# Performance work log

Measured on AMD Instinct MI355X. Metric: run time of the kernel, lower is better.

## Reference

```python
import jax, jax.numpy as jnp
import numpy as np

B, S, E, H = 4, 4096, 256, 2048
EPS = 1e-5

def layernorm(x, g, b):
    mu = jnp.mean(x, axis=-1, keepdims=True)
    var = jnp.mean(jnp.square(x - mu), axis=-1, keepdims=True)
    return (x - mu) * jax.lax.rsqrt(var + EPS) * g + b

def setup_inputs() -> dict:
    key = jax.random.key(0)
    ks = jax.random.split(key, 16)
    sE = 1.0 / np.sqrt(E)
    sH = 1.0 / np.sqrt(H)
    return {
        "x_embeddings": jax.random.normal(ks[0], (B, S, E), dtype=jnp.float32),
        "wq": jax.random.normal(ks[1], (E, E), dtype=jnp.float32) * sE,
        "bq": jnp.zeros((E,), jnp.float32),
        "wk": jax.random.normal(ks[2], (E, E), dtype=jnp.float32) * sE,
        "bk": jnp.zeros((E,), jnp.float32),
        "wv": jax.random.normal(ks[3], (E, E), dtype=jnp.float32) * sE,
        "bv": jnp.zeros((E,), jnp.float32),
        "w0": jax.random.normal(ks[4], (E, E), dtype=jnp.float32) * sE,
        "b0": jnp.zeros((E,), jnp.float32),
        "w1": jax.random.normal(ks[5], (E, H), dtype=jnp.float32) * sE,
        "b1": jnp.zeros((H,), jnp.float32),
        "ln_mlp_g": jnp.ones((H,), jnp.float32),
        "ln_mlp_b": jnp.zeros((H,), jnp.float32),
        "w2": jax.random.normal(ks[6], (H, E), dtype=jnp.float32) * sH,
        "b2": jnp.zeros((E,), jnp.float32),
        "ln1_g": jnp.ones((E,), jnp.float32),
        "ln1_b": jnp.zeros((E,), jnp.float32),
        "ln2_g": jnp.ones((E,), jnp.float32),
        "ln2_b": jnp.zeros((E,), jnp.float32),
    }

def reference(x_embeddings, wq, bq, wk, bk, wv, bv, w0, b0,
              w1, b1, ln_mlp_g, ln_mlp_b, w2, b2,
              ln1_g, ln1_b, ln2_g, ln2_b):
    x = x_embeddings
    q = x @ wq + bq
    k = x @ wk + bk
    v = x @ wv + bv
    # Unscaled, unmasked attention (faithful to source: no 1/sqrt(d), mask unused)
    scores = jnp.einsum('bqd,bkd->bqk', q, k)          # [B,S,S]
    probs = jax.nn.softmax(scores, axis=-1)
    attn = jnp.einsum('bqk,bkd->bqd', probs, v)        # [B,S,E]
    e = layernorm(x + attn, ln1_g, ln1_b) @ w0 + b0
    h = e @ w1 + b1                                     # [B,S,H]
    h = jax.nn.leaky_relu(layernorm(h, ln_mlp_g, ln_mlp_b))  # LnActivation: LN + LeakyReLU
    logits = h @ w2 + b2                                # [B,S,E]
    return layernorm(jax.nn.leaky_relu(logits + e), ln2_g, ln2_b)
```

## Files before the change

kernel.cpp:

```cpp
#include <hip/hip_runtime.h>

typedef unsigned short u16;
typedef unsigned int   u32;
typedef u16   u16x4 __attribute__((ext_vector_type(4)));
typedef u16   u16x8 __attribute__((ext_vector_type(8)));
typedef short s16x8 __attribute__((ext_vector_type(8)));
typedef float f32x4 __attribute__((ext_vector_type(4)));
typedef _Float16 f16x8 __attribute__((ext_vector_type(8)));

__device__ __forceinline__ u16 f2b(float f) {
  u32 u = __builtin_bit_cast(u32, f);
  u32 r = (u + 0x7fffu + ((u >> 16) & 1u)) >> 16;
  return (u16)r;
}
__device__ __forceinline__ float b2f(u16 h) {
  return __builtin_bit_cast(float, (u32)h << 16);
}
__device__ __forceinline__ u16 f2h(float f) {
  _Float16 h = (_Float16)f;
  return __builtin_bit_cast(u16, h);
}

__device__ __forceinline__ void async16(void* l, const void* g) {
  __builtin_amdgcn_global_load_lds((const __attribute__((address_space(1))) u32*)g,
                                   (__attribute__((address_space(3))) u32*)l, 16, 0, 0);
}

__device__ __forceinline__ float wave_sum(float v) {
#pragma unroll
  for (int m = 32; m; m >>= 1) v += __shfl_xor(v, m, 64);
  return v;
}

constexpr int BM = 128, BN = 128, BK = 64;

template<bool SPLIT, int OMODE>
__global__ __launch_bounds__(256)
void k_gemm_bt(const u16* __restrict__ Ah, const u16* __restrict__ Al, long lda,
               const u16* __restrict__ Bh, const u16* __restrict__ Bl, long ldb,
               const float* __restrict__ bias,
               float* __restrict__ Cf, u16* __restrict__ Cb, u16* __restrict__ Cl,
               long ldc, int K)
{
  __shared__ u16 lds[(SPLIT ? 4 : 2) * BM * BK];
  const int tid = threadIdx.x;
  const long arow0 = (long)blockIdx.y * BM;
  const long bcol0 = (long)blockIdx.x * BN;

  long offA[4], offB[4];
#pragma unroll
  for (int r = 0; r < 4; ++r) {
    const int off = r * 4096 + tid * 16;
    const int row = off >> 7;
    const int colb = off & 127;
    offA[r] = (arow0 + row) * lda + (colb >> 1);
    offB[r] = (bcol0 + row) * ldb + (colb >> 1);
  }

  const int lane = tid & 63;
  const int wid = tid >> 6;
  const int wr = (wid >> 1) * 64;
  const int wc = (wid & 1) * 64;
  const int fr = lane & 15;
  const int fk = (lane >> 4) * 8;

  f32x4 acc[4][4] = {};

  for (int k0 = 0; k0 < K; k0 += BK) {
#pragma unroll
    for (int r = 0; r < 4; ++r) {
      const int loff = (r * 4096 + tid * 16) >> 1;
      async16(&lds[loff],           Ah + offA[r] + k0);
      async16(&lds[BM*BK + loff],   Bh + offB[r] + k0);
      if constexpr (SPLIT) {
        async16(&lds[2*BM*BK + loff], Al + offA[r] + k0);
        async16(&lds[3*BM*BK + loff], Bl + offB[r] + k0);
      }
    }
    __syncthreads();
#pragma unroll
    for (int kk = 0; kk < BK; kk += 32) {
      s16x8 a[4], b[4];
#pragma unroll
      for (int m = 0; m < 4; ++m)
        a[m] = *(const s16x8*)&lds[(wr + m*16 + fr) * BK + kk + fk];
#pragma unroll
      for (int n = 0; n < 4; ++n)
        b[n] = *(const s16x8*)&lds[BM*BK + (wc + n*16 + fr) * BK + kk + fk];
#pragma unroll
      for (int m = 0; m < 4; ++m)
#pragma unroll
        for (int n = 0; n < 4; ++n)
          acc[m][n] = __builtin_amdgcn_mfma_f32_16x16x32_bf16(a[m], b[n], acc[m][n], 0, 0, 0);
      if constexpr (SPLIT) {
        s16x8 al[4], bl[4];
#pragma unroll
        for (int m = 0; m < 4; ++m)
          al[m] = *(const s16x8*)&lds[2*BM*BK + (wr + m*16 + fr) * BK + kk + fk];
#pragma unroll
        for (int n = 0; n < 4; ++n)
          bl[n] = *(const s16x8*)&lds[3*BM*BK + (wc + n*16 + fr) * BK + kk + fk];
#pragma unroll
        for (int m = 0; m < 4; ++m)
#pragma unroll
          for (int n = 0; n < 4; ++n) {
            acc[m][n] = __builtin_amdgcn_mfma_f32_16x16x32_bf16(a[m], bl[n], acc[m][n], 0, 0, 0);
            acc[m][n] = __builtin_amdgcn_mfma_f32_16x16x32_bf16(al[m], b[n], acc[m][n], 0, 0, 0);
          }
      }
    }
    __syncthreads();
  }

  float bv[4];
#pragma unroll
  for (int n = 0; n < 4; ++n) {
    const long gcol = bcol0 + wc + n*16 + fr;
    bv[n] = bias ? bias[gcol] : 0.f;
  }

#pragma unroll
  for (int m = 0; m < 4; ++m) {
#pragma unroll
    for (int reg = 0; reg < 4; ++reg) {
      const long grow = arow0 + wr + m*16 + (lane >> 4) * 4 + reg;
      const long ro = grow * ldc;
#pragma unroll
      for (int n = 0; n < 4; ++n) {
        const long gcol = bcol0 + wc + n*16 + fr;
        const float val = acc[m][n][reg] + bv[n];
        if constexpr (OMODE == 0) {
          Cf[ro + gcol] = val;
        } else if constexpr (OMODE == 1) {
          Cb[ro + gcol] = f2b(val);
        } else if constexpr (OMODE == 4) {
          Cb[ro + gcol] = f2h(val);
        } else if constexpr (OMODE == 5) {
          const int band = (int)(bcol0 >> 8);
          u16* dst = (band == 0) ? Cb : (band == 1) ? Cl : (u16*)Cf;
          const long lc = gcol - (long)band * 256;
          dst[grow * 256 + lc] = (band < 2) ? f2h(val) : f2b(val);
        } else {
          const u16 hb = f2b(val);
          Cb[ro + gcol] = hb;
          Cl[ro + gcol] = f2b(val - b2f(hb));
        }
      }
    }
  }
}

__global__ __launch_bounds__(256)
void k_flash(const u16* __restrict__ q16, const u16* __restrict__ k16,
             const u16* __restrict__ vt,
             u16* __restrict__ attn)
{
  __shared__ u16 lkh[2][32*256];
  __shared__ float lS[32*36];
  __shared__ u16 lP[32*40];
  __shared__ float lm[32], ll[32], lsc[32];

  const int tid = threadIdx.x;
  const int lane = tid & 63, wid = tid >> 6;
  const long bo = (long)blockIdx.y * 1048576;
  const long q0 = (long)blockIdx.x * 32;

  const int fr  = lane & 15;
  const int hi2 = lane >> 4;
  const int fk  = hi2 * 8;
  const int qh_sel = wid >> 1;
  const int kh_sel = wid & 1;

  f16x8 qf[8];
  {
    const u16* qp = q16 + bo + (q0 + qh_sel*16 + fr) * 256;
#pragma unroll
    for (int c = 0; c < 8; ++c)
      qf[c] = *(const f16x8*)(qp + c*32 + fk);
  }

  if (tid < 32) { lm[tid] = -1e30f; ll[tid] = 0.f; }
  f32x4 acc[2][4] = {};

  const char* kp = (const char*)(k16 + bo);
  const u16* vbase = vt + bo;

  auto STAGE = [&](int k0s, int b) {
#pragma unroll
    for (int r = 0; r < 4; ++r) {
      const int L = r*4096 + tid*16;
      const int row = L >> 9;
      const int colb = L & 511;
      const long gb = (long)(k0s + row)*512 + (colb ^ ((row & 7) << 4));
      async16((char*)lkh[b] + L, kp + gb);
    }
  };

  STAGE(0, 0);
  __syncthreads();

  int cur = 0;
  for (int k0 = 0; k0 < 4096; k0 += 32) {
    s16x8 vb[4];
#pragma unroll
    for (int j = 0; j < 4; ++j)
      vb[j] = *(const s16x8*)(vbase + (long)(wid*64 + j*16 + fr)*4096 + k0 + fk);

    if (k0 + 32 < 4096) STAGE(k0 + 32, cur ^ 1);

    f32x4 s0 = {};
    const int kc = kh_sel*16 + fr;
    const int swz = (kc & 7) << 4;
#pragma unroll
    for (int c = 0; c < 8; ++c) {
      const int o = (c*64 + hi2*16) ^ swz;
      const f16x8 bh = *(const f16x8*)((const char*)lkh[cur] + kc*512 + o);
      s0 = __builtin_amdgcn_mfma_f32_16x16x32_f16(qf[c], bh, s0, 0, 0, 0);
    }
#pragma unroll
    for (int r = 0; r < 4; ++r)
      lS[(qh_sel*16 + hi2*4 + r)*36 + kh_sel*16 + fr] = s0[r];
    __syncthreads();

    {
      const int sr = tid >> 3;
      const int sc = (tid & 7) * 4;
      const float4 sv = *(const float4*)&lS[sr*36 + sc];
      float tmx = fmaxf(fmaxf(sv.x, sv.y), fmaxf(sv.z, sv.w));
#pragma unroll
      for (int m = 1; m < 8; m <<= 1) tmx = fmaxf(tmx, __shfl_xor(tmx, m, 64));
      const float mold = lm[sr];
      const float mnew = fmaxf(mold, tmx);
      const float p0 = __expf(sv.x - mnew), p1 = __expf(sv.y - mnew);
      const float p2 = __expf(sv.z - mnew), p3 = __expf(sv.w - mnew);
      float ps = p0 + p1 + p2 + p3;
#pragma unroll
      for (int m = 1; m < 8; m <<= 1) ps += __shfl_xor(ps, m, 64);
      const float scale = __expf(mold - mnew);
      if ((tid & 7) == 0) {
        lm[sr] = mnew;
        ll[sr] = ll[sr] * scale + ps;
        lsc[sr] = scale;
      }
      u16x4 pb; pb[0]=f2b(p0); pb[1]=f2b(p1); pb[2]=f2b(p2); pb[3]=f2b(p3);
      *(u16x4*)&lP[sr*40 + sc] = pb;
    }
    __syncthreads();

#pragma unroll
    for (int qm = 0; qm < 2; ++qm)
#pragma unroll
      for (int r = 0; r < 4; ++r) {
        const float s = lsc[qm*16 + hi2*4 + r];
#pragma unroll
        for (int j = 0; j < 4; ++j) acc[qm][j][r] *= s;
      }
#pragma unroll
    for (int qm = 0; qm < 2; ++qm) {
      const s16x8 pa = *(const s16x8*)&lP[(qm*16 + fr)*40 + fk];
#pragma unroll
      for (int j = 0; j < 4; ++j)
        acc[qm][j] = __builtin_amdgcn_mfma_f32_16x16x32_bf16(pa, vb[j], acc[qm][j], 0, 0, 0);
    }
    cur ^= 1;
  }

  __syncthreads();
#pragma unroll
  for (int qm = 0; qm < 2; ++qm)
#pragma unroll
    for (int r = 0; r < 4; ++r) {
      const int row = qm*16 + hi2*4 + r;
      const float inv = 1.0f / ll[row];
      u16* op = attn + bo + (q0 + row)*256 + wid*64 + fr;
#pragma unroll
      for (int j = 0; j < 4; ++j)
        op[j*16] = f2b(acc[qm][j][r] * inv);
    }
}


__global__ __launch_bounds__(256)
void k_split_cast(const float* __restrict__ in, u16* __restrict__ hi, u16* __restrict__ lo, long n4) {
  long i = (long)blockIdx.x * 256 + threadIdx.x;
  if (i >= n4) return;
  float4 v = ((const float4*)in)[i];
  float vv[4] = {v.x, v.y, v.z, v.w};
  u16x4 h, l;
#pragma unroll
  for (int j = 0; j < 4; ++j) {
    u16 hb = f2b(vv[j]);
    h[j] = hb;
    l[j] = f2b(vv[j] - b2f(hb));
  }
  ((u16x4*)hi)[i] = h;
  ((u16x4*)lo)[i] = l;
}

__global__ __launch_bounds__(256)
void k_transpose_qkv0(const float* __restrict__ wq, const float* __restrict__ wk,
                      const float* __restrict__ wv, const float* __restrict__ w0,
                      u16* __restrict__ catT_h, u16* __restrict__ catT_l,
                      u16* __restrict__ w0T,
                      const float* __restrict__ bq, const float* __restrict__ bk,
                      const float* __restrict__ bv, float* __restrict__ catBias) {
  __shared__ float t[32][33];
  const int z = blockIdx.z;
  const float* in = (z == 0) ? wq : (z == 1) ? wk : (z == 2) ? wv : w0;
  const int c0 = blockIdx.x * 32, r0 = blockIdx.y * 32;
  const int tx = threadIdx.x, ty = threadIdx.y;
#pragma unroll
  for (int i = 0; i < 4; ++i)
    t[ty + i*8][tx] = in[(long)(r0 + ty + i*8) * 256 + c0 + tx];
  __syncthreads();
#pragma unroll
  for (int i = 0; i < 4; ++i) {
    const float f = t[tx][ty + i*8];
    const u16 hb = f2b(f);
    if (z < 3) {
      const long o = (long)(z*256 + c0 + ty + i*8) * 256 + r0 + tx;
      catT_h[o] = hb;
      catT_l[o] = f2b(f - b2f(hb));
    } else {
      w0T[(long)(c0 + ty + i*8) * 256 + r0 + tx] = hb;
    }
  }
  if (z == 3 && blockIdx.x == 0 && blockIdx.y == 0) {
    const int t0 = ty * 32 + tx;
    catBias[t0] = bq[t0];
    catBias[256 + t0] = bk[t0];
    catBias[512 + t0] = bv[t0];
  }
}

__global__ __launch_bounds__(256)
void k_transpose_f32ns(const float* __restrict__ in, u16* __restrict__ hi, int R, int C) {
  __shared__ float t[32][33];
  const int c0 = blockIdx.x * 32, r0 = blockIdx.y * 32;
  const int tx = threadIdx.x, ty = threadIdx.y;
#pragma unroll
  for (int i = 0; i < 4; ++i)
    t[ty + i*8][tx] = in[(long)(r0 + ty + i*8) * C + c0 + tx];
  __syncthreads();
#pragma unroll
  for (int i = 0; i < 4; ++i)
    hi[(long)(c0 + ty + i*8) * R + r0 + tx] = f2b(t[tx][ty + i*8]);
}

__global__ __launch_bounds__(256)
void k_transpose_bf16(const u16* __restrict__ in, u16* __restrict__ out,
                      int R, int C, long sIn, long sOut) {
  __shared__ u16 t[32][34];
  const int z = blockIdx.z;
  const u16* ib = in + (long)z * sIn;
  u16* ob = out + (long)z * sOut;
  const int c0 = blockIdx.x * 32, r0 = blockIdx.y * 32;
  const int tx = threadIdx.x, ty = threadIdx.y;
#pragma unroll
  for (int i = 0; i < 4; ++i)
    t[ty + i*8][tx] = ib[(long)(r0 + ty + i*8) * C + c0 + tx];
  __syncthreads();
#pragma unroll
  for (int i = 0; i < 4; ++i)
    ob[(long)(c0 + ty + i*8) * R + r0 + tx] = t[tx][ty + i*8];
}

__global__ __launch_bounds__(256)
void k_add_ln(const float* __restrict__ x, const u16* __restrict__ a,
              const float* __restrict__ g, const float* __restrict__ b,
              u16* __restrict__ out) {
  const long row = (long)blockIdx.x * 4 + (threadIdx.x >> 6);
  const int lane = threadIdx.x & 63;
  const long base = row * 256 + lane * 4;
  const float4 xv = *(const float4*)(x + base);
  const u16x4 av = *(const u16x4*)(a + base);
  float t[4] = {xv.x + b2f(av[0]), xv.y + b2f(av[1]), xv.z + b2f(av[2]), xv.w + b2f(av[3])};
  float s = t[0] + t[1] + t[2] + t[3];
  float q = t[0]*t[0] + t[1]*t[1] + t[2]*t[2] + t[3]*t[3];
  s = wave_sum(s); q = wave_sum(q);
  const float mu = s * (1.f / 256.f);
  const float var = q * (1.f / 256.f) - mu * mu;
  const float rs = rsqrtf(var + 1e-5f);
  const float4 gv = *(const float4*)(g + lane * 4);
  const float4 bv = *(const float4*)(b + lane * 4);
  u16x4 o;
  o[0] = f2b((t[0] - mu) * rs * gv.x + bv.x);
  o[1] = f2b((t[1] - mu) * rs * gv.y + bv.y);
  o[2] = f2b((t[2] - mu) * rs * gv.z + bv.z);
  o[3] = f2b((t[3] - mu) * rs * gv.w + bv.w);
  *(u16x4*)(out + base) = o;
}

__global__ __launch_bounds__(256)
void k_ln_leaky(const u16* __restrict__ h, const float* __restrict__ g,
                const float* __restrict__ b, u16* __restrict__ out) {
  const long row = blockIdx.x;
  const int tid = threadIdx.x;
  const int lane = tid & 63, wid = tid >> 6;
  const u16x8 hv = *(const u16x8*)(h + row * 2048 + tid * 8);
  float f[8];
  float s = 0.f, q = 0.f;
#pragma unroll
  for (int j = 0; j < 8; ++j) { f[j] = b2f(hv[j]); s += f[j]; q += f[j] * f[j]; }
  s = wave_sum(s); q = wave_sum(q);
  __shared__ float rs_[4], rq_[4];
  if (lane == 0) { rs_[wid] = s; rq_[wid] = q; }
  __syncthreads();
  s = rs_[0] + rs_[1] + rs_[2] + rs_[3];
  q = rq_[0] + rq_[1] + rq_[2] + rq_[3];
  const float mu = s * (1.f / 2048.f);
  const float var = q * (1.f / 2048.f) - mu * mu;
  const float rsq = rsqrtf(var + 1e-5f);
  const float4 g0 = *(const float4*)(g + tid * 8);
  const float4 g1 = *(const float4*)(g + tid * 8 + 4);
  const float4 b0 = *(const float4*)(b + tid * 8);
  const float4 b1 = *(const float4*)(b + tid * 8 + 4);
  const float gg[8] = {g0.x, g0.y, g0.z, g0.w, g1.x, g1.y, g1.z, g1.w};
  const float bb[8] = {b0.x, b0.y, b0.z, b0.w, b1.x, b1.y, b1.z, b1.w};
  u16x8 o;
#pragma unroll
  for (int j = 0; j < 8; ++j) {
    float y = (f[j] - mu) * rsq * gg[j] + bb[j];
    y = y > 0.f ? y : 0.01f * y;
    o[j] = f2b(y);
  }
  *(u16x8*)(out + row * 2048 + tid * 8) = o;
}

__global__ __launch_bounds__(256)
void k_final(const float* __restrict__ lg, const u16* __restrict__ e,
             const float* __restrict__ g, const float* __restrict__ b,
             float* __restrict__ out) {
  const long row = (long)blockIdx.x * 4 + (threadIdx.x >> 6);
  const int lane = threadIdx.x & 63;
  const long base = row * 256 + lane * 4;
  const float4 lv = *(const float4*)(lg + base);
  const u16x4 ev = *(const u16x4*)(e + base);
  float t[4] = {lv.x + b2f(ev[0]), lv.y + b2f(ev[1]), lv.z + b2f(ev[2]), lv.w + b2f(ev[3])};
#pragma unroll
  for (int j = 0; j < 4; ++j) t[j] = t[j] > 0.f ? t[j] : 0.01f * t[j];
  float s = t[0] + t[1] + t[2] + t[3];
  float q = t[0]*t[0] + t[1]*t[1] + t[2]*t[2] + t[3]*t[3];
  s = wave_sum(s); q = wave_sum(q);
  const float mu = s * (1.f / 256.f);
  const float var = q * (1.f / 256.f) - mu * mu;
  const float rs = rsqrtf(var + 1e-5f);
  const float4 gv = *(const float4*)(g + lane * 4);
  const float4 bv = *(const float4*)(b + lane * 4);
  float4 o;
  o.x = (t[0] - mu) * rs * gv.x + bv.x;
  o.y = (t[1] - mu) * rs * gv.y + bv.y;
  o.z = (t[2] - mu) * rs * gv.z + bv.z;
  o.w = (t[3] - mu) * rs * gv.w + bv.w;
  *(float4*)(out + base) = o;
}


extern "C" void kernel_launch(void* const* d_in, const int* in_sizes, int n_in,
                              void* d_out, int out_size, void* d_ws, size_t ws_size,
                              hipStream_t stream) {
  const float* x   = (const float*)d_in[0];
  const float* wq  = (const float*)d_in[1];
  const float* bq  = (const float*)d_in[2];
  const float* wk  = (const float*)d_in[3];
  const float* bk  = (const float*)d_in[4];
  const float* wv  = (const float*)d_in[5];
  const float* bv_ = (const float*)d_in[6];
  const float* w0  = (const float*)d_in[7];
  const float* b0  = (const float*)d_in[8];
  const float* w1  = (const float*)d_in[9];
  const float* b1  = (const float*)d_in[10];
  const float* lmg = (const float*)d_in[11];
  const float* lmb = (const float*)d_in[12];
  const float* w2  = (const float*)d_in[13];
  const float* b2  = (const float*)d_in[14];
  const float* l1g = (const float*)d_in[15];
  const float* l1b = (const float*)d_in[16];
  const float* l2g = (const float*)d_in[17];
  const float* l2b = (const float*)d_in[18];

  char* ws = (char*)d_ws;
  float* out = (float*)d_out;

  u16* q16    = (u16*)(ws + 0);
  u16* k16    = (u16*)(ws + 16777216);
  u16* vT     = (u16*)(ws + 33554432);
  u16* x_hi   = (u16*)(ws + 41943040);
  u16* x_lo   = (u16*)(ws + 50331648);
  u16* v_b    = (u16*)(ws + 58720256);
  u16* attn_b = (u16*)(ws + 67108864);
  u16* ln1    = (u16*)(ws + 75497472);
  u16* e_b    = (u16*)(ws + 83886080);
  float* logits = (float*)(ws + 92274688);
  u16* h_b    = (u16*)(ws + 0);
  u16* catT_h = (u16*)(ws + 109051904);
  u16* catT_l = (u16*)(ws + 109445120);
  u16* w0T    = (u16*)(ws + 109838336);
  u16* w1T    = (u16*)(ws + 109969408);
  u16* w2T    = (u16*)(ws + 111017984);
  float* catBias = (float*)(ws + 112066560);

  const dim3 t256(256);
  const dim3 tr(32, 8);

  k_split_cast<<<4096, t256, 0, stream>>>(x, x_hi, x_lo, 1048576);
  k_transpose_qkv0<<<dim3(8, 8, 4), tr, 0, stream>>>(
      wq, wk, wv, w0, catT_h, catT_l, w0T, bq, bk, bv_, catBias);
  k_transpose_f32ns<<<dim3(64, 8), tr, 0, stream>>>(w1, w1T, 256, 2048);
  k_transpose_f32ns<<<dim3(8, 64), tr, 0, stream>>>(w2, w2T, 2048, 256);

  k_gemm_bt<true, 5><<<dim3(6, 128), t256, 0, stream>>>(
      x_hi, x_lo, 256, catT_h, catT_l, 256, catBias,
      (float*)v_b, q16, k16, 256, 256);
  k_transpose_bf16<<<dim3(8, 128, 4), tr, 0, stream>>>(v_b, vT, 4096, 256, 1048576, 1048576);

  k_flash<<<dim3(128, 4), t256, 0, stream>>>(q16, k16, vT, attn_b);

  k_add_ln<<<4096, t256, 0, stream>>>(x, attn_b, l1g, l1b, ln1);

  k_gemm_bt<false, 1><<<dim3(2, 128), t256, 0, stream>>>(
      ln1, nullptr, 256, w0T, nullptr, 256, b0, nullptr, e_b, nullptr, 256, 256);
  k_gemm_bt<false, 1><<<dim3(16, 128), t256, 0, stream>>>(
      e_b, nullptr, 256, w1T, nullptr, 256, b1, nullptr, h_b, nullptr, 2048, 256);
  k_ln_leaky<<<16384, t256, 0, stream>>>(h_b, lmg, lmb, h_b);
  k_gemm_bt<false, 0><<<dim3(2, 128), t256, 0, stream>>>(
      h_b, nullptr, 2048, w2T, nullptr, 2048, b2, logits, nullptr, nullptr, 256, 2048);
  k_final<<<4096, t256, 0, stream>>>(logits, e_b, l2g, l2b, out);
}
```

Before: 365.9 us.

## Fuse fp32 split-cast into QKV GEMM and split flash QK accumulator chain

Result: no change. 364.6 us (-0.4%).

```diff
diff --git a/kernel.cpp b/kernel.cpp
--- a/kernel.cpp
+++ b/kernel.cpp
@@ -5,6 +5,7 @@
 typedef u16   u16x4 __attribute__((ext_vector_type(4)));
 typedef u16   u16x8 __attribute__((ext_vector_type(8)));
 typedef short s16x8 __attribute__((ext_vector_type(8)));
+typedef u32   u32x4 __attribute__((ext_vector_type(4)));
 typedef float f32x4 __attribute__((ext_vector_type(4)));
 typedef _Float16 f16x8 __attribute__((ext_vector_type(8)));
 
@@ -19,6 +20,9 @@
 __device__ __forceinline__ u16 f2h(float f) {
   _Float16 h = (_Float16)f;
   return __builtin_bit_cast(u16, h);
+}
+__device__ __forceinline__ u32 cvtpk(float a, float b) {
+  u32 r; asm("v_cvt_pk_bf16_f32 %0, %1, %2" : "=v"(r) : "v"(a), "v"(b)); return r;
 }
 
 __device__ __forceinline__ void async16(void* l, const void* g) {
@@ -131,20 +135,122 @@
         const float val = acc[m][n][reg] + bv[n];
         if constexpr (OMODE == 0) {
           Cf[ro + gcol] = val;
-        } else if constexpr (OMODE == 1) {
+        } else {
           Cb[ro + gcol] = f2b(val);
-        } else if constexpr (OMODE == 4) {
-          Cb[ro + gcol] = f2h(val);
-        } else if constexpr (OMODE == 5) {
-          const int band = (int)(bcol0 >> 8);
-          u16* dst = (band == 0) ? Cb : (band == 1) ? Cl : (u16*)Cf;
-          const long lc = gcol - (long)band * 256;
-          dst[grow * 256 + lc] = (band < 2) ? f2h(val) : f2b(val);
-        } else {
-          const u16 hb = f2b(val);
-          Cb[ro + gcol] = hb;
-          Cl[ro + gcol] = f2b(val - b2f(hb));
         }
+      }
+    }
+  }
+}
+
+__global__ __launch_bounds__(256)
+void k_gemm_qkv(const float* __restrict__ Af,
+                const u16* __restrict__ Bh, const u16* __restrict__ Bl,
+                const float* __restrict__ bias,
+                u16* __restrict__ Cq, u16* __restrict__ Ck, u16* __restrict__ Cv)
+{
+  __shared__ float ldsA[BM * BK];
+  __shared__ u16 ldsBh[BN * BK];
+  __shared__ u16 ldsBl[BN * BK];
+  const int tid = threadIdx.x;
+  const long arow0 = (long)blockIdx.y * BM;
+  const long bcol0 = (long)blockIdx.x * BN;
+
+  long offA[8];
+#pragma unroll
+  for (int r = 0; r < 8; ++r) {
+    const int off = r * 4096 + tid * 16;
+    const int row = off >> 8;
+    const int colb = off & 255;
+    offA[r] = (arow0 + row) * 256 + (colb >> 2);
+  }
+  long offB[4];
+#pragma unroll
+  for (int r = 0; r < 4; ++r) {
+    const int off = r * 4096 + tid * 16;
+    const int row = off >> 7;
+    const int colb = off & 127;
+    offB[r] = (bcol0 + row) * 256 + (colb >> 1);
+  }
+
+  const int lane = tid & 63;
+  const int wid = tid >> 6;
+  const int wr = (wid >> 1) * 64;
+  const int wc = (wid & 1) * 64;
+  const int fr = lane & 15;
+  const int fk = (lane >> 4) * 8;
+
+  f32x4 acc[4][4] = {};
+
+  for (int k0 = 0; k0 < 256; k0 += BK) {
+#pragma unroll
+    for (int r = 0; r < 8; ++r)
+      async16((char*)ldsA + r*4096 + tid*16, Af + offA[r] + k0);
+#pragma unroll
+    for (int r = 0; r < 4; ++r) {
+      const int loff = (r * 4096 + tid * 16) >> 1;
+      async16(&ldsBh[loff], Bh + offB[r] + k0);
+      async16(&ldsBl[loff], Bl + offB[r] + k0);
+    }
+    __syncthreads();
+#pragma unroll
+    for (int kk = 0; kk < BK; kk += 32) {
+      s16x8 a[4], al[4];
+#pragma unroll
+      for (int m = 0; m < 4; ++m) {
+        const float* ap = &ldsA[(wr + m*16 + fr) * BK + kk + fk];
+        const float4 v0 = *(const float4*)ap;
+        const float4 v1 = *(const float4*)(ap + 4);
+        u32x4 H, L;
+        H[0] = cvtpk(v0.x, v0.y); H[1] = cvtpk(v0.z, v0.w);
+        H[2] = cvtpk(v1.x, v1.y); H[3] = cvtpk(v1.z, v1.w);
+        L[0] = cvtpk(v0.x - __builtin_bit_cast(float, H[0] << 16),
+                     v0.y - __builtin_bit_cast(float, H[0] & 0xffff0000u));
+        L[1] = cvtpk(v0.z - __builtin_bit_cast(float, H[1] << 16),
+                     v0.w - __builtin_bit_cast(float, H[1] & 0xffff0000u));
+        L[2] = cvtpk(v1.x - __builtin_bit_cast(float, H[2] << 16),
+                     v1.y - __builtin_bit_cast(float, H[2] & 0xffff0000u));
+        L[3] = cvtpk(v1.z - __builtin_bit_cast(float, H[3] << 16),
+                     v1.w - __builtin_bit_cast(float, H[3] & 0xffff0000u));
+        a[m]  = __builtin_bit_cast(s16x8, H);
+        al[m] = __builtin_bit_cast(s16x8, L);
+      }
+      s16x8 b[4], bl[4];
+#pragma unroll
+      for (int n = 0; n < 4; ++n) {
+        b[n]  = *(const s16x8*)&ldsBh[(wc + n*16 + fr) * BK + kk + fk];
+        bl[n] = *(const s16x8*)&ldsBl[(wc + n*16 + fr) * BK + kk + fk];
+      }
+#pragma unroll
+      for (int m = 0; m < 4; ++m)
+#pragma unroll
+        for (int n = 0; n < 4; ++n) {
+          acc[m][n] = __builtin_amdgcn_mfma_f32_16x16x32_bf16(a[m],  b[n],  acc[m][n], 0, 0, 0);
+          acc[m][n] = __builtin_amdgcn_mfma_f32_16x16x32_bf16(a[m],  bl[n], acc[m][n], 0, 0, 0);
+          acc[m][n] = __builtin_amdgcn_mfma_f32_16x16x32_bf16(al[m], b[n],  acc[m][n], 0, 0, 0);
+        }
+    }
+    __syncthreads();
+  }
+
+  float bv[4];
+#pragma unroll
+  for (int n = 0; n < 4; ++n)
+    bv[n] = bias[bcol0 + wc + n*16 + fr];
+
+  const int band = (int)(bcol0 >> 8);
+  u16* dst = (band == 0) ? Cq : (band == 1) ? Ck : Cv;
+
+#pragma unroll
+  for (int m = 0; m < 4; ++m) {
+#pragma unroll
+    for (int reg = 0; reg < 4; ++reg) {
+      const long grow = arow0 + wr + m*16 + (lane >> 4) * 4 + reg;
+#pragma unroll
+      for (int n = 0; n < 4; ++n) {
+        const long lc = bcol0 - (long)band*256 + wc + n*16 + fr;
+        const float val = acc[m][n][reg] + bv[n];
+        dst[grow * 256 + lc] = (band < 2) ? f2h(val) : f2b(val);
       }
     }
   }
@@ -208,15 +314,19 @@
 
     if (k0 + 32 < 4096) STAGE(k0 + 32, cur ^ 1);
 
-    f32x4 s0 = {};
+    f32x4 sa = {}, sb = {};
     const int kc = kh_sel*16 + fr;
     const int swz = (kc & 7) << 4;
 #pragma unroll
-    for (int c = 0; c < 8; ++c) {
-      const int o = (c*64 + hi2*16) ^ swz;
-      const f16x8 bh = *(const f16x8*)((const char*)lkh[cur] + kc*512 + o);
-      s0 = __builtin_amdgcn_mfma_f32_16x16x32_f16(qf[c], bh, s0, 0, 0, 0);
-    }
+    for (int c = 0; c < 4; ++c) {
+      const int o0 = ((2*c)*64 + hi2*16) ^ swz;
+      const int o1 = ((2*c + 1)*64 + hi2*16) ^ swz;
+      const f16x8 b0 = *(const f16x8*)((const char*)lkh[cur] + kc*512 + o0);
+      const f16x8 b1 = *(const f16x8*)((const char*)lkh[cur] + kc*512 + o1);
+      sa = __builtin_amdgcn_mfma_f32_16x16x32_f16(qf[2*c],     b0, sa, 0, 0, 0);
+      sb = __builtin_amdgcn_mfma_f32_16x16x32_f16(qf[2*c + 1], b1, sb, 0, 0, 0);
+    }
+    const f32x4 s0 = sa + sb;
 #pragma unroll
     for (int r = 0; r < 4; ++r)
       lS[(qh_sel*16 + hi2*4 + r)*36 + kh_sel*16 + fr] = s0[r];
@@ -279,23 +389,6 @@
     }
 }
 
-
-__global__ __launch_bounds__(256)
-void k_split_cast(const float* __restrict__ in, u16* __restrict__ hi, u16* __restrict__ lo, long n4) {
-  long i = (long)blockIdx.x * 256 + threadIdx.x;
-  if (i >= n4) return;
-  float4 v = ((const float4*)in)[i];
-  float vv[4] = {v.x, v.y, v.z, v.w};
-  u16x4 h, l;
-#pragma unroll
-  for (int j = 0; j < 4; ++j) {
-    u16 hb = f2b(vv[j]);
-    h[j] = hb;
-    l[j] = f2b(vv[j] - b2f(hb));
-  }
-  ((u16x4*)hi)[i] = h;
-  ((u16x4*)lo)[i] = l;
-}
 
 __global__ __launch_bounds__(256)
 void k_transpose_qkv0(const float* __restrict__ wq, const float* __restrict__ wk,
@@ -485,8 +578,6 @@
   u16* q16    = (u16*)(ws + 0);
   u16* k16    = (u16*)(ws + 16777216);
   u16* vT     = (u16*)(ws + 33554432);
-  u16* x_hi   = (u16*)(ws + 41943040);
-  u16* x_lo   = (u16*)(ws + 50331648);
   u16* v_b    = (u16*)(ws + 58720256);
   u16* attn_b = (u16*)(ws + 67108864);
   u16* ln1    = (u16*)(ws + 75497472);
@@ -503,15 +594,13 @@
   const dim3 t256(256);
   const dim3 tr(32, 8);
 
-  k_split_cast<<<4096, t256, 0, stream>>>(x, x_hi, x_lo, 1048576);
   k_transpose_qkv0<<<dim3(8, 8, 4), tr, 0, stream>>>(
       wq, wk, wv, w0, catT_h, catT_l, w0T, bq, bk, bv_, catBias);
   k_transpose_f32ns<<<dim3(64, 8), tr, 0, stream>>>(w1, w1T, 256, 2048);
   k_transpose_f32ns<<<dim3(8, 64), tr, 0, stream>>>(w2, w2T, 2048, 256);
 
-  k_gemm_bt<true, 5><<<dim3(6, 128), t256, 0, stream>>>(
-      x_hi, x_lo, 256, catT_h, catT_l, 256, catBias,
-      (float*)v_b, q16, k16, 256, 256);
+  k_gemm_qkv<<<dim3(6, 128), t256, 0, stream>>>(
+      x, catT_h, catT_l, catBias, q16, k16, v_b);
   k_transpose_bf16<<<dim3(8, 128, 4), tr, 0, stream>>>(v_b, vT, 4096, 256, 1048576, 1048576);
 
   k_flash<<<dim3(128, 4), t256, 0, stream>>>(q16, k16, vT, attn_b);
```
